# Performance work log

Hardware: AMD Instinct MI355X
Metric: run time of the kernel (lower is better)

## Reference

```python
import math
import jax, jax.numpy as jnp
import numpy as np

BH, S, DK = 64, 1024, 64   # batch*heads, seq_len, head dim
FG, FL = 32, 32            # global / local enrichment feature dims
H, B = 16, 4               # mask layout [heads, batch, seq]


def setup_inputs() -> dict:
    key = jax.random.key(0)
    k1, k2, k3, k4, k5, k6 = jax.random.split(key, 6)
    return {
        "query": jax.random.normal(k1, (BH, S, DK), dtype=jnp.float32),
        "key": jax.random.normal(k2, (BH, S, DK), dtype=jnp.float32),
        "value": jax.random.normal(k3, (BH, S, DK), dtype=jnp.float32),
        "local_f": jax.random.normal(k4, (BH, S, FL), dtype=jnp.float32),
        "global_f": jax.random.normal(k5, (BH, S, FG), dtype=jnp.float32),
        "mask": jax.random.randint(k6, (H, B, S), 0, 2, dtype=jnp.int32),
    }


def reference(query, key, value, local_f, global_f, mask):
    dk = query.shape[-1]
    # enrich q/k with global then local features (matches torch concat order)
    pq = jnp.concatenate([query, global_f, local_f], axis=2)   # [BH, S, dk+fg+fl]
    pk = jnp.concatenate([key, global_f, local_f], axis=2)
    scores = jnp.einsum("bqd,bkd->bqk", pq, pk) / math.sqrt(dk)  # [BH, S, S]
    # mask [H, B, S] -> [H*B, S] -> broadcast over query positions
    m = mask.reshape(-1, mask.shape[-1])[:, None, :]            # [H*B, 1, S]
    scores = jnp.where(m == 1, jnp.float32(-1e9), scores)
    attn = jax.nn.softmax(scores, axis=-1)
    return jnp.einsum("bqk,bkd->bqd", attn, value)              # [BH, S, dk]
```

## Files before the change

### kernel.cpp

```cpp
#include <hip/hip_runtime.h>
#include <hip/hip_bf16.h>


#define BHn 64
#define Sn  1024
#define NT  16
#define KSTR 152
#define VSTR 72
#define KTILE (64*KSTR*2)
#define VTILE (64*VSTR*2)
#define BUFSZ (KTILE+VTILE)
#define OSTR 68
#define WAIT_VM0 0x0F70

typedef __attribute__((ext_vector_type(8)))  __bf16 bf16x8;
typedef __attribute__((ext_vector_type(16))) float  f32x16;
typedef __attribute__((ext_vector_type(4)))  unsigned int u32x4;

__device__ __forceinline__ unsigned f2bf1(float a){
    union { float f; unsigned u; } c; c.f = a;
    return (c.u + 0x7fffu + ((c.u >> 16) & 1u)) >> 16;
}
__device__ __forceinline__ unsigned f2bf2(float a, float b){
    return f2bf1(a) | (f2bf1(b) << 16);
}
__device__ __forceinline__ unsigned pkbf(float a, float b){
    return __builtin_amdgcn_perm(__builtin_bit_cast(unsigned, b),
                                 __builtin_bit_cast(unsigned, a), 0x07060302u);
}
__device__ __forceinline__ void gld_lds16(const void* g, void* l){
    __builtin_amdgcn_global_load_lds(
        (const __attribute__((address_space(1))) unsigned int*)g,
        (__attribute__((address_space(3))) unsigned int*)l, 16, 0, 0);
}

__global__ __launch_bounds__(256)
void attn_prep(const float* __restrict__ K, const float* __restrict__ V,
               const float* __restrict__ LF, const float* __restrict__ GF,
               const int* __restrict__ M,
               unsigned short* __restrict__ Kp, unsigned short* __restrict__ Vp)
{
    const int tid = threadIdx.x;
    const int bh = blockIdx.x >> 4, ti = blockIdx.x & 15, kb = ti*64;
    unsigned short* ktg = Kp + (size_t)(bh*NT + ti) * (64*KSTR);
    unsigned int*   vtg = (unsigned int*)(Vp + (size_t)(bh*NT + ti) * (64*VSTR));

    #pragma unroll
    for (int i=0;i<2;i++){
        int idx = tid + 256*i, row = idx>>3, c = idx&7;
        const float* s = K + ((size_t)bh*Sn + kb + row)*64 + c*8;
        float4 f0 = *(const float4*)s, f1 = *(const float4*)(s+4);
        u32x4 w; w[0]=f2bf2(f0.x,f0.y); w[1]=f2bf2(f0.z,f0.w);
        w[2]=f2bf2(f1.x,f1.y); w[3]=f2bf2(f1.z,f1.w);
        *(u32x4*)(ktg + row*KSTR + c*8) = w;
    }
    {
        int row = tid>>2, c = tid&3;
        const float* s = GF + ((size_t)bh*Sn + kb + row)*32 + c*8;
        float4 f0 = *(const float4*)s, f1 = *(const float4*)(s+4);
        u32x4 w; w[0]=f2bf2(f0.x,f0.y); w[1]=f2bf2(f0.z,f0.w);
        w[2]=f2bf2(f1.x,f1.y); w[3]=f2bf2(f1.z,f1.w);
        *(u32x4*)(ktg + row*KSTR + 64 + c*8) = w;
    }
    {
        int row = tid>>2, c = tid&3;
        const float* s = LF + ((size_t)bh*Sn + kb + row)*32 + c*8;
        float4 f0 = *(const float4*)s, f1 = *(const float4*)(s+4);
        u32x4 w; w[0]=f2bf2(f0.x,f0.y); w[1]=f2bf2(f0.z,f0.w);
        w[2]=f2bf2(f1.x,f1.y); w[3]=f2bf2(f1.z,f1.w);
        *(u32x4*)(ktg + row*KSTR + 96 + c*8) = w;
    }
    if (tid < 64){
        int mv = M[(size_t)bh*Sn + kb + tid];
        u32x4 w; w[0] = (mv == 1) ? 0x0000ceacu : 0u;
        w[1]=0u; w[2]=0u; w[3]=0u;
        *(u32x4*)(ktg + tid*KSTR + 128) = w;
        u32x4 z; z[0]=0u; z[1]=0u; z[2]=0u; z[3]=0u;
        *(u32x4*)(ktg + tid*KSTR + 136) = z;
        *(u32x4*)(ktg + tid*KSTR + 144) = z;
    }
    {
        int d = tid & 63, g = tid >> 6;
        const float* vb = V + ((size_t)bh*Sn + kb + 16*g)*64 + d;
        const int pm[16] = {0,1,2,3, 8,9,10,11, 4,5,6,7, 12,13,14,15};
        unsigned w[8];
        #pragma unroll
        for (int m=0;m<8;m++)
            w[m] = f2bf2(vb[(size_t)pm[2*m]*64], vb[(size_t)pm[2*m+1]*64]);
        u32x4 a, b;
        a[0]=w[0]; a[1]=w[1]; a[2]=w[2]; a[3]=w[3];
        b[0]=w[4]; b[1]=w[5]; b[2]=w[6]; b[3]=w[7];
        *(u32x4*)(vtg + d*36 + g*8)     = a;
        *(u32x4*)(vtg + d*36 + g*8 + 4) = b;
    }
}

__global__ __launch_bounds__(512, 4)
void attn_main(const float* __restrict__ Q, const unsigned short* __restrict__ Kp,
               const unsigned short* __restrict__ Vp,
               const float* __restrict__ GF, const float* __restrict__ LF,
               float* __restrict__ O)
{
    __shared__ __align__(16) unsigned char smem[2*BUFSZ];
    const int tid  = threadIdx.x;
    const int wave = tid >> 6, lane = tid & 63;
    const int l31  = lane & 31, h = lane >> 5;
    const int qh   = wave >> 1;
    const int kp   = wave & 1;
    const int bh = blockIdx.x & 63;
    const int qb = blockIdx.x >> 6;
    const float SCL = 0.18033688011112042f;

    const int qrow = qb*128 + qh*32 + l31;
    u32x4 qf[9];
    #pragma unroll
    for (int dc = 0; dc < 8; dc++){
        const int cb = dc*16 + 8*h;
        const float* src;
        if (cb < 64)      src = Q  + ((size_t)bh*Sn + qrow)*64 + cb;
        else if (cb < 96) src = GF + ((size_t)bh*Sn + qrow)*32 + (cb - 64);
        else              src = LF + ((size_t)bh*Sn + qrow)*32 + (cb - 96);
        float4 f0 = *(const float4*)src;
        float4 f1 = *(const float4*)(src + 4);
        qf[dc][0] = f2bf2(f0.x*SCL, f0.y*SCL);
        qf[dc][1] = f2bf2(f0.z*SCL, f0.w*SCL);
        qf[dc][2] = f2bf2(f1.x*SCL, f1.y*SCL);
        qf[dc][3] = f2bf2(f1.z*SCL, f1.w*SCL);
    }
    qf[8][0] = h ? 0u : 0x00003f80u;
    qf[8][1] = 0u; qf[8][2] = 0u; qf[8][3] = 0u;

    f32x16 oacc[2];
    #pragma unroll
    for (int dt=0; dt<2; dt++)
        #pragma unroll
        for (int r=0; r<16; r++) oacc[dt][r] = 0.f;
    float lrun = 0.f;

    const unsigned char* gKb = (const unsigned char*)Kp + (size_t)bh*NT*KTILE;
    const unsigned char* gVb = (const unsigned char*)Vp + (size_t)bh*NT*VTILE;

    {
        #pragma unroll
        for (int i=0;i<4;i++){
            int c = wave + 8*i;
            if (c < 19)      gld_lds16(gKb + (size_t)c*1024 + lane*16, smem + c*1024);
            else if (c < 28) gld_lds16(gVb + (size_t)(c-19)*1024 + lane*16,
                                       smem + KTILE + (size_t)(c-19)*1024);
        }
    }
    __builtin_amdgcn_s_waitcnt(WAIT_VM0);

    for (int t = 0; t < NT; t++){
        unsigned char* cur = smem + (size_t)(t&1)*BUFSZ;
        unsigned char* nxt = smem + (size_t)((t+1)&1)*BUFSZ;
        __syncthreads();
        if (t+1 < NT){
            const unsigned char* gK = gKb + (size_t)(t+1)*KTILE;
            const unsigned char* gV = gVb + (size_t)(t+1)*VTILE;
            #pragma unroll
            for (int i=0;i<4;i++){
                int c = wave + 8*i;
                if (c < 19)      gld_lds16(gK + (size_t)c*1024 + lane*16, nxt + c*1024);
                else if (c < 28) gld_lds16(gV + (size_t)(c-19)*1024 + lane*16,
                                           nxt + KTILE + (size_t)(c-19)*1024);
            }
        }
        unsigned short* kt_s = (unsigned short*)cur;
        unsigned short* vt_s = (unsigned short*)(cur + KTILE);

        f32x16 acc;
        #pragma unroll
        for (int r=0;r<16;r++) acc[r] = 0.f;
        #pragma unroll
        for (int dc=0; dc<9; dc++){
            u32x4 ar = *(const u32x4*)(kt_s + (kp*32 + l31)*KSTR + dc*16 + 8*h);
            acc = __builtin_amdgcn_mfma_f32_32x32x16_bf16(
                    __builtin_bit_cast(bf16x8, ar),
                    __builtin_bit_cast(bf16x8, qf[dc]), acc, 0, 0, 0);
        }

        float rs = 0.f;
        #pragma unroll
        for (int r=0;r<16;r++){
            float p = __builtin_amdgcn_exp2f(acc[r]);
            acc[r] = p; rs += p;
        }
        lrun += rs;

        unsigned pk[8];
        #pragma unroll
        for (int i=0;i<8;i++) pk[i] = pkbf(acc[2*i], acc[2*i+1]);
        u32x4 b0, b1;
        b0[0]=pk[0]; b0[1]=pk[1]; b0[2]=pk[2]; b0[3]=pk[3];
        b1[0]=pk[4]; b1[1]=pk[5]; b1[2]=pk[6]; b1[3]=pk[7];

        #pragma unroll
        for (int dt=0;dt<2;dt++){
            u32x4 va0 = *(const u32x4*)(vt_s + (dt*32 + l31)*VSTR + kp*32 + 8*h);
            u32x4 va1 = *(const u32x4*)(vt_s + (dt*32 + l31)*VSTR + kp*32 + 16 + 8*h);
            oacc[dt] = __builtin_amdgcn_mfma_f32_32x32x16_bf16(
                    __builtin_bit_cast(bf16x8, va0),
                    __builtin_bit_cast(bf16x8, b0), oacc[dt], 0, 0, 0);
            oacc[dt] = __builtin_amdgcn_mfma_f32_32x32x16_bf16(
                    __builtin_bit_cast(bf16x8, va1),
                    __builtin_bit_cast(bf16x8, b1), oacc[dt], 0, 0, 0);
        }

        __builtin_amdgcn_s_waitcnt(WAIT_VM0);
    }

    __syncthreads();
    float lw = lrun + __shfl_xor(lrun, 32, 64);
    float* s1 = (float*)smem;
    float* s2 = (float*)(smem + 128*OSTR*4);
    if (kp == 1){
        #pragma unroll
        for (int dt=0;dt<2;dt++)
            #pragma unroll
            for (int rg=0;rg<4;rg++){
                float4 w;
                w.x = oacc[dt][rg*4+0]; w.y = oacc[dt][rg*4+1];
                w.z = oacc[dt][rg*4+2]; w.w = oacc[dt][rg*4+3];
                *(float4*)(s1 + (qh*32 + l31)*OSTR + dt*32 + rg*8 + 4*h) = w;
            }
        if (h == 0) s2[qh*32 + l31] = lw;
    }
    __syncthreads();
    if (kp == 0){
        float inv = 1.0f / (lw + s2[qh*32 + l31]);
        #pragma unroll
        for (int dt=0;dt<2;dt++)
            #pragma unroll
            for (int rg=0;rg<4;rg++){
                float* p = s1 + (qh*32 + l31)*OSTR + dt*32 + rg*8 + 4*h;
                float4 w = *(float4*)p;
                w.x = (w.x + oacc[dt][rg*4+0])*inv;
                w.y = (w.y + oacc[dt][rg*4+1])*inv;
                w.z = (w.z + oacc[dt][rg*4+2])*inv;
                w.w = (w.w + oacc[dt][rg*4+3])*inv;
                *(float4*)p = w;
            }
    }
    __syncthreads();
    #pragma unroll
    for (int i=0;i<4;i++){
        int idx = tid + 512*i, r = idx>>4, c = idx&15;
        *(float4*)(O + ((size_t)bh*Sn + qb*128 + r)*64 + c*4) =
            *(const float4*)(s1 + r*OSTR + c*4);
    }
}

extern "C" void kernel_launch(void* const* d_in, const int* in_sizes, int n_in,
                              void* d_out, int out_size, void* d_ws, size_t ws_size,
                              hipStream_t stream) {
    const float* Q  = (const float*)d_in[0];
    const float* K  = (const float*)d_in[1];
    const float* V  = (const float*)d_in[2];
    const float* LF = (const float*)d_in[3];
    const float* GF = (const float*)d_in[4];
    const int*   M  = (const int*)d_in[5];
    float* O = (float*)d_out;

    unsigned short* Kp = (unsigned short*)d_ws;
    unsigned short* Vp = Kp + (size_t)BHn*NT*64*KSTR;

    attn_prep<<<dim3(BHn*NT), dim3(256), 0, stream>>>(K, V, LF, GF, M, Kp, Vp);
    attn_main<<<dim3(BHn*(Sn/128)), dim3(512), 0, stream>>>(Q, Kp, Vp, GF, LF, O);
}
```

Baseline: 143.5 us.

## Halve block to 256 threads, each wave computing two 32-row query subtiles

Each wave now handles two 32-query subtiles that share the same K and V fragments read from LDS, and the block shrinks from 8 to 4 waves while still covering 128 query rows. The goal is to halve LDS reads of K/V per MFMA and raise per-wave instruction-level parallelism with two independent accumulator chains. The cost is higher register pressure (doubled Q fragments and output accumulators) and fewer waves per block for latency hiding. The tile-load loop is redistributed across 4 waves, 7 chunks each.

```diff
diff --git a/kernel.cpp b/kernel.cpp
--- a/kernel.cpp
+++ b/kernel.cpp
@@ -95,7 +95,7 @@
     }
 }
 
-__global__ __launch_bounds__(512, 4)
+__global__ __launch_bounds__(256, 2)
 void attn_main(const float* __restrict__ Q, const unsigned short* __restrict__ Kp,
                const unsigned short* __restrict__ Vp,
                const float* __restrict__ GF, const float* __restrict__ LF,
@@ -105,49 +105,52 @@
     const int tid  = threadIdx.x;
     const int wave = tid >> 6, lane = tid & 63;
     const int l31  = lane & 31, h = lane >> 5;
-    const int qh   = wave >> 1;
+    const int qh2  = wave >> 1;
     const int kp   = wave & 1;
     const int bh = blockIdx.x & 63;
     const int qb = blockIdx.x >> 6;
     const float SCL = 0.18033688011112042f;
 
-    const int qrow = qb*128 + qh*32 + l31;
-    u32x4 qf[9];
-    #pragma unroll
-    for (int dc = 0; dc < 8; dc++){
-        const int cb = dc*16 + 8*h;
-        const float* src;
-        if (cb < 64)      src = Q  + ((size_t)bh*Sn + qrow)*64 + cb;
-        else if (cb < 96) src = GF + ((size_t)bh*Sn + qrow)*32 + (cb - 64);
-        else              src = LF + ((size_t)bh*Sn + qrow)*32 + (cb - 96);
-        float4 f0 = *(const float4*)src;
-        float4 f1 = *(const float4*)(src + 4);
-        qf[dc][0] = f2bf2(f0.x*SCL, f0.y*SCL);
-        qf[dc][1] = f2bf2(f0.z*SCL, f0.w*SCL);
-        qf[dc][2] = f2bf2(f1.x*SCL, f1.y*SCL);
-        qf[dc][3] = f2bf2(f1.z*SCL, f1.w*SCL);
-    }
-    qf[8][0] = h ? 0u : 0x00003f80u;
-    qf[8][1] = 0u; qf[8][2] = 0u; qf[8][3] = 0u;
-
-    f32x16 oacc[2];
-    #pragma unroll
-    for (int dt=0; dt<2; dt++)
-        #pragma unroll
-        for (int r=0; r<16; r++) oacc[dt][r] = 0.f;
-    float lrun = 0.f;
+    u32x4 qf[2][9];
+    #pragma unroll
+    for (int sub=0; sub<2; sub++){
+        const int qrow = qb*128 + qh2*64 + sub*32 + l31;
+        #pragma unroll
+        for (int dc = 0; dc < 8; dc++){
+            const int cb = dc*16 + 8*h;
+            const float* src;
+            if (cb < 64)      src = Q  + ((size_t)bh*Sn + qrow)*64 + cb;
+            else if (cb < 96) src = GF + ((size_t)bh*Sn + qrow)*32 + (cb - 64);
+            else              src = LF + ((size_t)bh*Sn + qrow)*32 + (cb - 96);
+            float4 f0 = *(const float4*)src;
+            float4 f1 = *(const float4*)(src + 4);
+            qf[sub][dc][0] = f2bf2(f0.x*SCL, f0.y*SCL);
+            qf[sub][dc][1] = f2bf2(f0.z*SCL, f0.w*SCL);
+            qf[sub][dc][2] = f2bf2(f1.x*SCL, f1.y*SCL);
+            qf[sub][dc][3] = f2bf2(f1.z*SCL, f1.w*SCL);
+        }
+        qf[sub][8][0] = h ? 0u : 0x00003f80u;
+        qf[sub][8][1] = 0u; qf[sub][8][2] = 0u; qf[sub][8][3] = 0u;
+    }
+
+    f32x16 oacc[2][2];
+    #pragma unroll
+    for (int s=0;s<2;s++)
+        #pragma unroll
+        for (int dt=0;dt<2;dt++)
+            #pragma unroll
+            for (int r=0;r<16;r++) oacc[s][dt][r] = 0.f;
+    float lrun0 = 0.f, lrun1 = 0.f;
 
     const unsigned char* gKb = (const unsigned char*)Kp + (size_t)bh*NT*KTILE;
     const unsigned char* gVb = (const unsigned char*)Vp + (size_t)bh*NT*VTILE;
 
-    {
-        #pragma unroll
-        for (int i=0;i<4;i++){
-            int c = wave + 8*i;
-            if (c < 19)      gld_lds16(gKb + (size_t)c*1024 + lane*16, smem + c*1024);
-            else if (c < 28) gld_lds16(gVb + (size_t)(c-19)*1024 + lane*16,
-                                       smem + KTILE + (size_t)(c-19)*1024);
-        }
+    #pragma unroll
+    for (int i=0;i<7;i++){
+        int c = wave*7 + i;
+        if (c < 19) gld_lds16(gKb + (size_t)c*1024 + lane*16, smem + c*1024);
+        else        gld_lds16(gVb + (size_t)(c-19)*1024 + lane*16,
+                              smem + KTILE + (size_t)(c-19)*1024);
     }
     __builtin_amdgcn_s_waitcnt(WAIT_VM0);
 
@@ -159,93 +162,115 @@
             const unsigned char* gK = gKb + (size_t)(t+1)*KTILE;
             const unsigned char* gV = gVb + (size_t)(t+1)*VTILE;
             #pragma unroll
-            for (int i=0;i<4;i++){
-                int c = wave + 8*i;
-                if (c < 19)      gld_lds16(gK + (size_t)c*1024 + lane*16, nxt + c*1024);
-                else if (c < 28) gld_lds16(gV + (size_t)(c-19)*1024 + lane*16,
-                                           nxt + KTILE + (size_t)(c-19)*1024);
+            for (int i=0;i<7;i++){
+                int c = wave*7 + i;
+                if (c < 19) gld_lds16(gK + (size_t)c*1024 + lane*16, nxt + c*1024);
+                else        gld_lds16(gV + (size_t)(c-19)*1024 + lane*16,
+                                      nxt + KTILE + (size_t)(c-19)*1024);
             }
         }
         unsigned short* kt_s = (unsigned short*)cur;
         unsigned short* vt_s = (unsigned short*)(cur + KTILE);
 
-        f32x16 acc;
-        #pragma unroll
-        for (int r=0;r<16;r++) acc[r] = 0.f;
+        f32x16 acc0, acc1;
+        #pragma unroll
+        for (int r=0;r<16;r++){ acc0[r] = 0.f; acc1[r] = 0.f; }
         #pragma unroll
         for (int dc=0; dc<9; dc++){
             u32x4 ar = *(const u32x4*)(kt_s + (kp*32 + l31)*KSTR + dc*16 + 8*h);
-            acc = __builtin_amdgcn_mfma_f32_32x32x16_bf16(
+            acc0 = __builtin_amdgcn_mfma_f32_32x32x16_bf16(
                     __builtin_bit_cast(bf16x8, ar),
-                    __builtin_bit_cast(bf16x8, qf[dc]), acc, 0, 0, 0);
-        }
-
-        float rs = 0.f;
+                    __builtin_bit_cast(bf16x8, qf[0][dc]), acc0, 0, 0, 0);
+            acc1 = __builtin_amdgcn_mfma_f32_32x32x16_bf16(
+                    __builtin_bit_cast(bf16x8, ar),
+                    __builtin_bit_cast(bf16x8, qf[1][dc]), acc1, 0, 0, 0);
+        }
+
+        float rs0 = 0.f, rs1 = 0.f;
         #pragma unroll
         for (int r=0;r<16;r++){
-            float p = __builtin_amdgcn_exp2f(acc[r]);
-            acc[r] = p; rs += p;
-        }
-        lrun += rs;
-
-        unsigned pk[8];
-        #pragma unroll
-        for (int i=0;i<8;i++) pk[i] = pkbf(acc[2*i], acc[2*i+1]);
-        u32x4 b0, b1;
-        b0[0]=pk[0]; b0[1]=pk[1]; b0[2]=pk[2]; b0[3]=pk[3];
-        b1[0]=pk[4]; b1[1]=pk[5]; b1[2]=pk[6]; b1[3]=pk[7];
+            float p0 = __builtin_amdgcn_exp2f(acc0[r]);
+            float p1 = __builtin_amdgcn_exp2f(acc1[r]);
+            acc0[r] = p0; rs0 += p0;
+            acc1[r] = p1; rs1 += p1;
+        }
+        lrun0 += rs0; lrun1 += rs1;
+
+        u32x4 b0s0, b1s0, b0s1, b1s1;
+        #pragma unroll
+        for (int i=0;i<4;i++){
+            b0s0[i] = pkbf(acc0[2*i],   acc0[2*i+1]);
+            b1s0[i] = pkbf(acc0[2*i+8], acc0[2*i+9]);
+            b0s1[i] = pkbf(acc1[2*i],   acc1[2*i+1]);
+            b1s1[i] = pkbf(acc1[2*i+8], acc1[2*i+9]);
+        }
 
         #pragma unroll
         for (int dt=0;dt<2;dt++){
             u32x4 va0 = *(const u32x4*)(vt_s + (dt*32 + l31)*VSTR + kp*32 + 8*h);
             u32x4 va1 = *(const u32x4*)(vt_s + (dt*32 + l31)*VSTR + kp*32 + 16 + 8*h);
-            oacc[dt] = __builtin_amdgcn_mfma_f32_32x32x16_bf16(
+            oacc[0][dt] = __builtin_amdgcn_mfma_f32_32x32x16_bf16(
                     __builtin_bit_cast(bf16x8, va0),
-                    __builtin_bit_cast(bf16x8, b0), oacc[dt], 0, 0, 0);
-            oacc[dt] = __builtin_amdgcn_mfma_f32_32x32x16_bf16(
+                    __builtin_bit_cast(bf16x8, b0s0), oacc[0][dt], 0, 0, 0);
+            oacc[0][dt] = __builtin_amdgcn_mfma_f32_32x32x16_bf16(
                     __builtin_bit_cast(bf16x8, va1),
-                    __builtin_bit_cast(bf16x8, b1), oacc[dt], 0, 0, 0);
+                    __builtin_bit_cast(bf16x8, b1s0), oacc[0][dt], 0, 0, 0);
+            oacc[1][dt] = __builtin_amdgcn_mfma_f32_32x32x16_bf16(
+                    __builtin_bit_cast(bf16x8, va0),
+                    __builtin_bit_cast(bf16x8, b0s1), oacc[1][dt], 0, 0, 0);
+            oacc[1][dt] = __builtin_amdgcn_mfma_f32_32x32x16_bf16(
+                    __builtin_bit_cast(bf16x8, va1),
+                    __builtin_bit_cast(bf16x8, b1s1), oacc[1][dt], 0, 0, 0);
         }
 
         __builtin_amdgcn_s_waitcnt(WAIT_VM0);
     }
 
     __syncthreads();
-    float lw = lrun + __shfl_xor(lrun, 32, 64);
+    float lw0 = lrun0 + __shfl_xor(lrun0, 32, 64);
+    float lw1 = lrun1 + __shfl_xor(lrun1, 32, 64);
     float* s1 = (float*)smem;
     float* s2 = (float*)(smem + 128*OSTR*4);
     if (kp == 1){
         #pragma unroll
-        for (int dt=0;dt<2;dt++)
-            #pragma unroll
-            for (int rg=0;rg<4;rg++){
-                float4 w;
-                w.x = oacc[dt][rg*4+0]; w.y = oacc[dt][rg*4+1];
-                w.z = oacc[dt][rg*4+2]; w.w = oacc[dt][rg*4+3];
-                *(float4*)(s1 + (qh*32 + l31)*OSTR + dt*32 + rg*8 + 4*h) = w;
-            }
-        if (h == 0) s2[qh*32 + l31] = lw;
+        for (int sub=0;sub<2;sub++){
+            int qr = qh2*64 + sub*32 + l31;
+            #pragma unroll
+            for (int dt=0;dt<2;dt++)
+                #pragma unroll
+                for (int rg=0;rg<4;rg++){
+                    float4 w;
+                    w.x = oacc[sub][dt][rg*4+0]; w.y = oacc[sub][dt][rg*4+1];
+                    w.z = oacc[sub][dt][rg*4+2]; w.w = oacc[sub][dt][rg*4+3];
+                    *(float4*)(s1 + qr*OSTR + dt*32 + rg*8 + 4*h) = w;
+                }
+            if (h == 0) s2[qr] = sub ? lw1 : lw0;
+        }
     }
     __syncthreads();
     if (kp == 0){
-        float inv = 1.0f / (lw + s2[qh*32 + l31]);
-        #pragma unroll
-        for (int dt=0;dt<2;dt++)
-            #pragma unroll
-            for (int rg=0;rg<4;rg++){
-                float* p = s1 + (qh*32 + l31)*OSTR + dt*32 + rg*8 + 4*h;
-                float4 w = *(float4*)p;
-                w.x = (w.x + oacc[dt][rg*4+0])*inv;
-                w.y = (w.y + oacc[dt][rg*4+1])*inv;
-                w.z = (w.z + oacc[dt][rg*4+2])*inv;
-                w.w = (w.w + oacc[dt][rg*4+3])*inv;
-                *(float4*)p = w;
-            }
+        #pragma unroll
+        for (int sub=0;sub<2;sub++){
+            int qr = qh2*64 + sub*32 + l31;
+            float inv = 1.0f / ((sub ? lw1 : lw0) + s2[qr]);
+            #pragma unroll
+            for (int dt=0;dt<2;dt++)
+                #pragma unroll
+                for (int rg=0;rg<4;rg++){
+                    float* p = s1 + qr*OSTR + dt*32 + rg*8 + 4*h;
+                    float4 w = *(float4*)p;
+                    w.x = (w.x + oacc[sub][dt][rg*4+0])*inv;
+                    w.y = (w.y + oacc[sub][dt][rg*4+1])*inv;
+                    w.z = (w.z + oacc[sub][dt][rg*4+2])*inv;
+                    w.w = (w.w + oacc[sub][dt][rg*4+3])*inv;
+                    *(float4*)p = w;
+                }
+        }
     }
     __syncthreads();
     #pragma unroll
-    for (int i=0;i<4;i++){
-        int idx = tid + 512*i, r = idx>>4, c = idx&15;
+    for (int i=0;i<8;i++){
+        int idx = tid + 256*i, r = idx>>4, c = idx&15;
         *(float4*)(O + ((size_t)bh*Sn + qb*128 + r)*64 + c*4) =
             *(const float4*)(s1 + r*OSTR + c*4);
     }
@@ -266,5 +291,5 @@
     unsigned short* Vp = Kp + (size_t)BHn*NT*64*KSTR;
 
     attn_prep<<<dim3(BHn*NT), dim3(256), 0, stream>>>(K, V, LF, GF, M, Kp, Vp);
-    attn_main<<<dim3(BHn*(Sn/128)), dim3(512), 0, stream>>>(Q, Kp, Vp, GF, LF, O);
-}
+    attn_main<<<dim3(BHn*(Sn/128)), dim3(256), 0, stream>>>(Q, Kp, Vp, GF, LF, O);
+}
```

New measurement: 145.7 us. Within noise of the previous version (+1.5%).
